# Kernel tuning notes

Hardware: AMD Instinct MI355X
Metric: run time of the kernel (lower is better)

The kernel has to match this reference:

```python
import jax, jax.numpy as jnp
import numpy as np

B, D, N, H = 16, 512, 4096, 4
HD = D // H  # head_dim = 128


def conv1(x, w, b):
    # 1x1 Conv1d == per-position matmul. x: (b, Cin, L), w: (Cout, Cin), b: (Cout,)
    return jnp.einsum('oi,bin->bon', w, x) + b[:, None]


def ln_c(x, g, b, eps=1e-5):
    # TransLN: LayerNorm over the channel axis (axis=1) at every position.
    m = jnp.mean(x, axis=1, keepdims=True)
    v = jnp.var(x, axis=1, keepdims=True)
    return (x - m) * jax.lax.rsqrt(v + eps) * g[:, None] + b[:, None]


def gelu(x):
    return jax.nn.gelu(x, approximate=False)  # torch nn.GELU default = exact erf


def setup_inputs() -> dict:
    key = jax.random.key(0)
    ks = iter(jax.random.split(key, 40))

    def rn(*shape):
        return jax.random.normal(next(ks), shape, jnp.float32) * 0.02

    inp = {
        'group_token': jax.random.normal(next(ks), (B, D, 2), jnp.float32),
        'x': jax.random.normal(next(ks), (B, D, N), jnp.float32),
        # mlp_s: Mlp(2, D//2) -> Conv1d(2, D//2), GELU, Conv1d(D//2, 2)
        'ws1_w': rn(D // 2, 2), 'ws1_b': jnp.zeros(D // 2, jnp.float32),
        'ws2_w': rn(2, D // 2), 'ws2_b': jnp.zeros(2, jnp.float32),
        # mlp_c: Mlp(D, 4D)
        'wc1_w': rn(4 * D, D), 'wc1_b': jnp.zeros(4 * D, jnp.float32),
        'wc2_w': rn(D, 4 * D), 'wc2_b': jnp.zeros(D, jnp.float32),
        # proj q/k/v: Conv1d(D, D)
        'q_w': rn(D, D), 'q_b': jnp.zeros(D, jnp.float32),
        'k_w': rn(D, D), 'k_b': jnp.zeros(D, jnp.float32),
        'v_w': rn(D, D), 'v_b': jnp.zeros(D, jnp.float32),
        'merge_w': rn(D, D), 'merge_b': jnp.zeros(D, jnp.float32),
        # mlp = MLP([2D, 2D, D], do_bn=False): Conv1d(2D,2D), GELU, Conv1d(2D,D)
        'm1_w': rn(2 * D, 2 * D), 'm1_b': jnp.zeros(2 * D, jnp.float32),
        'm2_w': rn(D, 2 * D), 'm2_b': jnp.zeros(D, jnp.float32),
        # norm0 / norm1 LayerNorm(D)
        'n0_g': jnp.ones(D, jnp.float32), 'n0_b': jnp.zeros(D, jnp.float32),
        'n1_g': jnp.ones(D, jnp.float32), 'n1_b': jnp.zeros(D, jnp.float32),
        # grouping: D->64->16->4->2 with TransLN+GELU between, softmax(axis=1)
        'g1_w': rn(64, D), 'g1_b': jnp.zeros(64, jnp.float32),
        'gl1_g': jnp.ones(64, jnp.float32), 'gl1_b': jnp.zeros(64, jnp.float32),
        'g2_w': rn(16, 64), 'g2_b': jnp.zeros(16, jnp.float32),
        'gl2_g': jnp.ones(16, jnp.float32), 'gl2_b': jnp.zeros(16, jnp.float32),
        'g3_w': rn(4, 16), 'g3_b': jnp.zeros(4, jnp.float32),
        'gl3_g': jnp.ones(4, jnp.float32), 'gl3_b': jnp.zeros(4, jnp.float32),
        'g4_w': rn(2, 4), 'g4_b': jnp.zeros(2, jnp.float32),
    }
    return inp


def reference(group_token, x, ws1_w, ws1_b, ws2_w, ws2_b, wc1_w, wc1_b, wc2_w, wc2_b,
              q_w, q_b, k_w, k_b, v_w, v_b, merge_w, merge_b,
              m1_w, m1_b, m2_w, m2_b, n0_g, n0_b, n1_g, n1_b,
              g1_w, g1_b, gl1_g, gl1_b, g2_w, g2_b, gl2_g, gl2_b,
              g3_w, g3_b, gl3_g, gl3_b, g4_w, g4_b):
    b = x.shape[0]
    # group_token: (b, D, 2)
    gt_t = jnp.swapaxes(group_token, 1, 2)                    # (b, 2, D)
    s = conv1(gelu(conv1(gt_t, ws1_w, ws1_b)), ws2_w, ws2_b)  # (b, 2, D)
    gt = group_token + jnp.swapaxes(s, 1, 2)
    gt = gt + conv1(gelu(conv1(gt, wc1_w, wc1_b)), wc2_w, wc2_b)

    # projections; torch view(b, head_dim, heads, -1) splits channels as (HD, H)
    q = conv1(x, q_w, q_b).reshape(b, HD, H, N)
    k = conv1(gt, k_w, k_b).reshape(b, HD, H, 2)
    v = conv1(gt, v_w, v_b).reshape(b, HD, H, 2)

    attn = jax.nn.softmax(jnp.einsum('bdhn,bdhm->bhnm', q, k) * (HD ** -0.5), axis=-1)
    out = jnp.einsum('bhnm,bdhm->bdhn', attn, v).reshape(b, D, N)
    out = conv1(out, merge_w, merge_b)

    h = jnp.concatenate([x, ln_c(out, n0_g, n0_b)], axis=1)   # (b, 2D, N)
    h = conv1(gelu(conv1(h, m1_w, m1_b)), m2_w, m2_b)         # (b, D, N)
    xd = x + ln_c(h, n1_g, n1_b)

    g = gelu(ln_c(conv1(xd, g1_w, g1_b), gl1_g, gl1_b))
    g = gelu(ln_c(conv1(g, g2_w, g2_b), gl2_g, gl2_b))
    g = gelu(ln_c(conv1(g, g3_w, g3_b), gl3_g, gl3_b))
    g = jax.nn.softmax(conv1(g, g4_w, g4_b), axis=1)          # (b, 2, N)
    return g[:, 0, :]                                         # (b, N)
```

## Files before the change

### kernel.cpp

```cpp
#include <hip/hip_runtime.h>
#include <math.h>

typedef unsigned short u16;
typedef unsigned int u32;
typedef __attribute__((ext_vector_type(8))) short bfrag;
typedef __attribute__((ext_vector_type(4))) float f32x4;

__device__ __forceinline__ float gelu_f(float x){
  float z = fabsf(x) * 0.70710678118654752440f;
  float t = __builtin_amdgcn_rcpf(1.0f + 0.3275911f*z);
  float p = t*(0.254829592f + t*(-0.284496736f + t*(1.421413741f
            + t*(-1.453152027f + t*1.061405429f))));
  float e = __expf(-z*z);
  float er = copysignf(1.0f - p*e, x);
  return 0.5f * x * (1.0f + er);
}
__device__ __forceinline__ u16 f2bf(float f){
  union { float f; unsigned int i; } c; c.f = f;
  unsigned int i = c.i;
  return (u16)((i + 0x7FFFu + ((i >> 16) & 1u)) >> 16);
}
__device__ __forceinline__ float bf2f(u16 u){
  union { unsigned int i; float f; } c; c.i = ((unsigned int)u) << 16; return c.f;
}

__device__ __forceinline__ void gload_lds16(const u16* g, u16* l){
  __builtin_amdgcn_global_load_lds(
      (const __attribute__((address_space(1))) u32*)(g),
      (__attribute__((address_space(3))) u32*)(l),
      16, 0, 0);
}

struct F8 { float v[8]; };
__device__ __forceinline__ F8 load8f(const float* p){
  float4 a = *(const float4*)p; float4 b = *(const float4*)(p + 4);
  F8 r; r.v[0]=a.x; r.v[1]=a.y; r.v[2]=a.z; r.v[3]=a.w;
  r.v[4]=b.x; r.v[5]=b.y; r.v[6]=b.z; r.v[7]=b.w; return r;
}

#define PRE_STRIDE 4624

__global__ __launch_bounds__(256) void k0a_mlps(
    const float* __restrict__ gtok,
    const float* __restrict__ ws1_w, const float* __restrict__ ws1_b,
    const float* __restrict__ ws2_w, const float* __restrict__ ws2_b,
    float* __restrict__ GT1)
{
  __shared__ float sw1[256][2]; __shared__ float sb1[256];
  __shared__ float sw2[2][256];
  const int b = blockIdx.x;
  const int t = threadIdx.x;
  sw1[t][0] = ws1_w[2*t]; sw1[t][1] = ws1_w[2*t+1];
  sb1[t] = ws1_b[t];
  sw2[0][t] = ws2_w[t]; sw2[1][t] = ws2_w[256+t];
  __syncthreads();
  const int j = blockIdx.y*256 + t;
  const float a0 = gtok[b*1024 + 2*j], a1 = gtok[b*1024 + 2*j + 1];
  float s0 = ws2_b[0], s1 = ws2_b[1];
  #pragma unroll 4
  for (int o = 0; o < 256; ++o){
    float h = gelu_f(sw1[o][0]*a0 + sw1[o][1]*a1 + sb1[o]);
    s0 += sw2[0][o]*h; s1 += sw2[1][o]*h;
  }
  GT1[b*1024 + 2*j]     = a0 + s0;
  GT1[b*1024 + 2*j + 1] = a1 + s1;
}

__global__ __launch_bounds__(256) void k0b_fc1(
    const float* __restrict__ GT1,
    const float* __restrict__ wc1_w, const float* __restrict__ wc1_b,
    float* __restrict__ HID)
{
  __shared__ float g[1024];
  const int b = blockIdx.x;
  const int t = threadIdx.x;
  for (int i = t; i < 1024; i += 256) g[i] = GT1[b*1024 + i];
  __syncthreads();
  const int o = blockIdx.y*256 + t;
  const float* wr = wc1_w + (size_t)o*512;
  float acc0 = wc1_b[o], acc1 = acc0;
  for (int d = 0; d < 512; d += 8){
    F8 w = load8f(wr + d);
    #pragma unroll
    for (int i = 0; i < 8; ++i){
      acc0 += w.v[i]*g[(d+i)*2];
      acc1 += w.v[i]*g[(d+i)*2+1];
    }
  }
  HID[b*4096 + o]        = gelu_f(acc0);
  HID[b*4096 + 2048 + o] = gelu_f(acc1);
}

__global__ __launch_bounds__(256) void k0c_fc2(
    const float* __restrict__ GT1, const float* __restrict__ HID,
    const float* __restrict__ wc2_w, const float* __restrict__ wc2_b,
    float* __restrict__ GT2)
{
  __shared__ float h0[2048], h1[2048];
  const int b = blockIdx.x;
  const int t = threadIdx.x;
  for (int i = t; i < 2048; i += 256){
    h0[i] = HID[b*4096 + i]; h1[i] = HID[b*4096 + 2048 + i];
  }
  __syncthreads();
  const int d = blockIdx.y*256 + t;
  const float* wr = wc2_w + (size_t)d*2048;
  float acc0 = wc2_b[d], acc1 = acc0;
  for (int o = 0; o < 2048; o += 8){
    F8 w = load8f(wr + o);
    #pragma unroll
    for (int i = 0; i < 8; ++i){
      acc0 += w.v[i]*h0[o+i];
      acc1 += w.v[i]*h1[o+i];
    }
  }
  GT2[b*1024 + 2*d]     = GT1[b*1024 + 2*d]     + acc0;
  GT2[b*1024 + 2*d + 1] = GT1[b*1024 + 2*d + 1] + acc1;
}

__global__ __launch_bounds__(256) void k0d_kv(
    const float* __restrict__ GT2,
    const float* __restrict__ k_w,
    const float* __restrict__ v_w, const float* __restrict__ v_b,
    float* __restrict__ DK, float* __restrict__ DV, float* __restrict__ V1L)
{
  __shared__ float g[1024];
  const int b = blockIdx.x;
  const int t = threadIdx.x;
  for (int i = t; i < 1024; i += 256) g[i] = GT2[b*1024 + i];
  __syncthreads();
  const int c = blockIdx.y*256 + t;
  const float* kr = k_w + (size_t)c*512;
  const float* vr = v_w + (size_t)c*512;
  float k0a=0.f,k1a=0.f,v0a=0.f,v1a=0.f;
  for (int d = 0; d < 512; d += 8){
    F8 kw = load8f(kr + d); F8 vw = load8f(vr + d);
    #pragma unroll
    for (int i = 0; i < 8; ++i){
      float g0 = g[(d+i)*2], g1 = g[(d+i)*2+1];
      k0a += kw.v[i]*g0; k1a += kw.v[i]*g1;
      v0a += vw.v[i]*g0; v1a += vw.v[i]*g1;
    }
  }
  DK[b*512 + c]  = k0a - k1a;
  DV[b*512 + c]  = v0a - v1a;
  V1L[b*512 + c] = v1a + v_b[c];
}

__global__ __launch_bounds__(256) void k0e_qpre(
    const float* __restrict__ DK,
    const float* __restrict__ q_w, const float* __restrict__ q_b,
    float* __restrict__ PRE)
{
  __shared__ float dkl[512];
  const int b = blockIdx.x;
  const int t = threadIdx.x;
  for (int i = t; i < 512; i += 256) dkl[i] = DK[b*512 + i];
  __syncthreads();
  const int i = blockIdx.y*256 + t;
  float w0=0.f,w1=0.f,w2=0.f,w3=0.f;
  for (int c = 0; c < 512; c += 4){
    w0 += dkl[c]  *q_w[(size_t)(c)  *512 + i];
    w1 += dkl[c+1]*q_w[(size_t)(c+1)*512 + i];
    w2 += dkl[c+2]*q_w[(size_t)(c+2)*512 + i];
    w3 += dkl[c+3]*q_w[(size_t)(c+3)*512 + i];
  }
  float* P = PRE + (size_t)b * PRE_STRIDE;
  P[0*512+i]=w0; P[1*512+i]=w1; P[2*512+i]=w2; P[3*512+i]=w3;
  if (blockIdx.y == 0 && t < 4){
    float bsum = 0.f;
    for (int c = t; c < 512; c += 4) bsum += dkl[c]*q_b[c];
    P[2048 + t] = bsum;
  }
}

__global__ __launch_bounds__(256) void k0f_mpre(
    const float* __restrict__ DV, const float* __restrict__ V1L,
    const float* __restrict__ merge_w, const float* __restrict__ merge_b,
    float* __restrict__ PRE)
{
  __shared__ float dvl[512], v1ll[512];
  const int b = blockIdx.x;
  const int t = threadIdx.x;
  for (int i = t; i < 512; i += 256){
    dvl[i] = DV[b*512 + i]; v1ll[i] = V1L[b*512 + i];
  }
  __syncthreads();
  const int r = blockIdx.y*256 + t;
  const float* mw = merge_w + (size_t)r*512;
  float ab = merge_b[r];
  float mh[4] = {0.f,0.f,0.f,0.f};
  for (int c = 0; c < 512; c += 8){
    F8 w = load8f(mw + c);
    #pragma unroll
    for (int i = 0; i < 8; ++i){
      ab += w.v[i]*v1ll[c+i];
      mh[i&3] += w.v[i]*dvl[c+i];
    }
  }
  float* P = PRE + (size_t)b * PRE_STRIDE;
  P[2064 + r] = ab;
  *(float4*)&P[2576 + r*4] = make_float4(mh[0],mh[1],mh[2],mh[3]);
}

__global__ __launch_bounds__(256) void kcvt(const float* __restrict__ s,
                                            u16* __restrict__ d, int n8)
{
  int g = blockIdx.x*256 + threadIdx.x;
  if (g >= n8) return;
  F8 v = load8f(s + (size_t)g*8);
  u16 o[8];
  #pragma unroll
  for (int i=0;i<8;++i) o[i] = f2bf(v.v[i]);
  *(uint4*)(d + (size_t)g*8) = *(uint4*)o;
}

__global__ __launch_bounds__(256) void kcvt_dup(const float* __restrict__ g1w,
                                                u16* __restrict__ out)
{
  int idx = blockIdx.x*256 + threadIdx.x;
  int r = idx >> 10, k = idx & 1023;
  out[idx] = f2bf(g1w[r*512 + (k & 511)]);
}

__global__ __launch_bounds__(256) void k1_fused(
    const float* __restrict__ x, const float* __restrict__ PRE,
    const float* __restrict__ n0_g, const float* __restrict__ n0_b,
    int j0_global, u16* __restrict__ XYbT)
{
  __shared__ float wd[4][512];
  __shared__ float bs[512];
  __shared__ float Mm[512][4];
  __shared__ float gam[512], bet[512];
  __shared__ float beta4[4];
  __shared__ float part[4][4][64];
  __shared__ float pstat[2][4][64];
  const int tid = threadIdx.x;
  const int cid = tid & 63;
  const int qtr = tid >> 6;
  const int jl = blockIdx.x*64 + cid;
  const int jg = j0_global + jl;
  const int b = jg >> 12, n = jg & 4095;
  const float* P = PRE + (size_t)b * PRE_STRIDE;
  for (int i = tid; i < 2048; i += 256) wd[i>>9][i&511] = P[i];
  if (tid < 4) beta4[tid] = P[2048 + tid];
  for (int i = tid; i < 512; i += 256){
    bs[i] = P[2064 + i]; gam[i] = n0_g[i]; bet[i] = n0_b[i];
  }
  for (int i = tid; i < 2048; i += 256) Mm[i>>2][i&3] = P[2576 + i];
  __syncthreads();
  const float* xc = x + (size_t)b*2097152 + n;
  u16* col = XYbT + (size_t)jl*1024;
  const int ibase = qtr*128;
  float l0=0.f, l1=0.f, l2=0.f, l3=0.f;
  for (int i0 = 0; i0 < 128; i0 += 32){
    u16 ob[32];
    #pragma unroll
    for (int m = 0; m < 32; ++m){
      int i = ibase + i0 + m;
      float xv = xc[(size_t)i*4096];
      ob[m] = f2bf(xv);
      l0 += wd[0][i]*xv; l1 += wd[1][i]*xv;
      l2 += wd[2][i]*xv; l3 += wd[3][i]*xv;
    }
    #pragma unroll
    for (int q = 0; q < 4; ++q)
      *(uint4*)&col[ibase + i0 + 8*q] = *(uint4*)&ob[8*q];
  }
  part[0][qtr][cid] = l0; part[1][qtr][cid] = l1;
  part[2][qtr][cid] = l2; part[3][qtr][cid] = l3;
  __syncthreads();
  l0 = part[0][0][cid] + part[0][1][cid] + part[0][2][cid] + part[0][3][cid] + beta4[0];
  l1 = part[1][0][cid] + part[1][1][cid] + part[1][2][cid] + part[1][3][cid] + beta4[1];
  l2 = part[2][0][cid] + part[2][1][cid] + part[2][2][cid] + part[2][3][cid] + beta4[2];
  l3 = part[3][0][cid] + part[3][1][cid] + part[3][2][cid] + part[3][3][cid] + beta4[3];
  const float sc = 0.0883883476483184405f;
  float p0 = 1.f/(1.f+expf(-sc*l0));
  float p1 = 1.f/(1.f+expf(-sc*l1));
  float p2 = 1.f/(1.f+expf(-sc*l2));
  float p3 = 1.f/(1.f+expf(-sc*l3));
  float s=0.f, s2=0.f;
  for (int c = ibase; c < ibase + 128; ++c){
    float m = bs[c] + Mm[c][0]*p0 + Mm[c][1]*p1 + Mm[c][2]*p2 + Mm[c][3]*p3;
    s += m; s2 += m*m;
  }
  pstat[0][qtr][cid] = s; pstat[1][qtr][cid] = s2;
  __syncthreads();
  s  = pstat[0][0][cid] + pstat[0][1][cid] + pstat[0][2][cid] + pstat[0][3][cid];
  s2 = pstat[1][0][cid] + pstat[1][1][cid] + pstat[1][2][cid] + pstat[1][3][cid];
  float mean = s*(1.f/512.f);
  float rs = rsqrtf(s2*(1.f/512.f) - mean*mean + 1e-5f);
  for (int c0 = 0; c0 < 128; c0 += 32){
    u16 ob[32];
    #pragma unroll
    for (int m = 0; m < 32; ++m){
      int c = ibase + c0 + m;
      float v = bs[c] + Mm[c][0]*p0 + Mm[c][1]*p1 + Mm[c][2]*p2 + Mm[c][3]*p3;
      ob[m] = f2bf((v - mean)*rs*gam[c] + bet[c]);
    }
    #pragma unroll
    for (int q = 0; q < 4; ++q)
      *(uint4*)&col[512 + ibase + c0 + 8*q] = *(uint4*)&ob[8*q];
  }
}

__global__ __launch_bounds__(256) void mfma_gemm_p(
    const u16* __restrict__ Wb, const float* __restrict__ bias,
    const u16* __restrict__ XT, int K, int M,
    u16* __restrict__ Out, int do_gelu, int log2nbi)
{
  __shared__ __align__(16) u16 SH[3][8192];
  const int tid = threadIdx.x;
  const int lane = tid & 63;
  const int wv = __builtin_amdgcn_readfirstlane(tid >> 6);
  const int id = blockIdx.x;
  const int bi = (id >> 3) & ((1 << log2nbi) - 1);
  const int bj = (id & 7) + 8 * (id >> (3 + log2nbi));
  const int roff = (wv >> 1) * 64;
  const int noff = (wv & 1) * 64;
  const int lm = lane & 15, quad = lane >> 4;
  const int qs = (quad ^ ((lm >> 1) & 3)) * 8;

  f32x4 acc[4][4];
  #pragma unroll
  for (int i=0;i<4;++i){
    #pragma unroll
    for (int j=0;j<4;++j) acc[i][j] = (f32x4){0.f,0.f,0.f,0.f};
  }

  const int r16 = lane >> 2;
  const int kc  = (((lane & 3) ^ ((lane >> 3) & 3))) * 8;
  const u16* aG = Wb + (size_t)(bi*128 + wv*32 + r16)*K + kc;
  const u16* bG = XT + (size_t)(bj*128 + wv*32 + r16)*1024 + kc;
  const int aOff = wv*1024;
  const int bOff = 4096 + wv*1024;

#define GP_STAGE(base, kk) do { \
    gload_lds16(aG + (kk),                 (base) + aOff); \
    gload_lds16(aG + (size_t)16*K + (kk),  (base) + aOff + 512); \
    gload_lds16(bG + (kk),                 (base) + bOff); \
    gload_lds16(bG + 16*1024 + (kk),       (base) + bOff + 512); \
  } while(0)

#define GP_COMPUTE(base) do { \
    bfrag av[4], bv[4]; \
    _Pragma("unroll") \
    for (int i=0;i<4;++i) \
      av[i] = *(const bfrag*)&(base)[(roff + 16*i + lm)*32 + qs]; \
    _Pragma("unroll") \
    for (int j=0;j<4;++j) \
      bv[j] = *(const bfrag*)&(base)[4096 + (noff + 16*j + lm)*32 + qs]; \
    __builtin_amdgcn_s_setprio(1); \
    _Pragma("unroll") \
    for (int i=0;i<4;++i){ \
      _Pragma("unroll") \
      for (int j=0;j<4;++j) \
        acc[i][j] = __builtin_amdgcn_mfma_f32_16x16x32_bf16(av[i], bv[j], acc[i][j], 0,0,0); \
    } \
    __builtin_amdgcn_s_setprio(0); \
  } while(0)

  u16* b0 = &SH[0][0];
  u16* b1 = &SH[1][0];
  u16* b2 = &SH[2][0];
  GP_STAGE(b0, 0);
  GP_STAGE(b1, 32);
  for (int k0 = 0; k0 + 64 < K; k0 += 32){
    GP_STAGE(b2, k0 + 64);
    asm volatile("s_waitcnt vmcnt(8)" ::: "memory");
    __builtin_amdgcn_s_barrier();
    __builtin_amdgcn_sched_barrier(0);
    GP_COMPUTE(b0);
    __builtin_amdgcn_sched_barrier(0);
    __builtin_amdgcn_s_barrier();
    u16* t = b0; b0 = b1; b1 = b2; b2 = t;
  }
  asm volatile("s_waitcnt vmcnt(4)" ::: "memory");
  __builtin_amdgcn_s_barrier();
  __builtin_amdgcn_sched_barrier(0);
  GP_COMPUTE(b0);
  asm volatile("s_waitcnt vmcnt(0)" ::: "memory");
  __builtin_amdgcn_s_barrier();
  __builtin_amdgcn_sched_barrier(0);
  GP_COMPUTE(b1);
  __syncthreads();
#undef GP_STAGE
#undef GP_COMPUTE

  u16* Tt = &SH[0][0];
  #pragma unroll
  for (int i=0;i<4;++i){
    float4 bb = *(const float4*)&bias[bi*128 + roff + 16*i + quad*4];
    float b4[4] = {bb.x,bb.y,bb.z,bb.w};
    #pragma unroll
    for (int j=0;j<4;++j){
      int colr = noff + 16*j + lm;
      #pragma unroll
      for (int s2=0;s2<2;++s2){
        float v0 = acc[i][j][2*s2]   + b4[2*s2];
        float v1 = acc[i][j][2*s2+1] + b4[2*s2+1];
        if (do_gelu){ v0 = gelu_f(v0); v1 = gelu_f(v1); }
        unsigned int dw = (unsigned int)f2bf(v0) | ((unsigned int)f2bf(v1) << 16);
        *(unsigned int*)&Tt[colr*136 + roff + 16*i + quad*4 + 2*s2] = dw;
      }
    }
  }
  __syncthreads();
  {
    int c = tid >> 1, q = tid & 1;
    u16* dst = Out + (size_t)(bj*128 + c)*M + bi*128 + q*64;
    const u16* src = &Tt[c*136 + q*64];
    #pragma unroll
    for (int m=0;m<8;++m)
      *(uint4*)(dst + m*8) = *(const uint4*)(src + m*8);
  }
}

__global__ __launch_bounds__(256) void mfma_g64h(
    const u16* __restrict__ Wg, const float* __restrict__ bias,
    const u16* __restrict__ XT,
    const float* __restrict__ gl1_g, const float* __restrict__ gl1_b,
    const float* __restrict__ g2_w, const float* __restrict__ g2_b,
    const float* __restrict__ gl2_g, const float* __restrict__ gl2_b,
    const float* __restrict__ g3_w, const float* __restrict__ g3_b,
    const float* __restrict__ gl3_g, const float* __restrict__ gl3_b,
    const float* __restrict__ g4_w, const float* __restrict__ g4_b, int has_g4b,
    float* __restrict__ Outp, int j0_global)
{
  __shared__ __align__(16) u16 SH[3][6144];
  const int tid = threadIdx.x;
  const int lane = tid & 63;
  const int wv = __builtin_amdgcn_readfirstlane(tid >> 6);
  const int bj = blockIdx.x;
  const int lm = lane & 15, quad = lane >> 4;
  const int qs = (quad ^ ((lm >> 1) & 3)) * 8;

  f32x4 acc[4][2];
  #pragma unroll
  for (int i=0;i<4;++i){
    #pragma unroll
    for (int j=0;j<2;++j) acc[i][j] = (f32x4){0.f,0.f,0.f,0.f};
  }
  const int r16 = lane >> 2;
  const int kc  = (((lane & 3) ^ ((lane >> 3) & 3))) * 8;
  const u16* aG = Wg + (size_t)(wv*16 + r16)*1024 + kc;
  const u16* bG = XT + (size_t)(bj*128 + wv*32 + r16)*1024 + kc;
  const int aOff = wv*512;
  const int bOff = 2048 + wv*1024;

#define G64_STAGE(base, kk) do { \
    gload_lds16(aG + (kk),             (base) + aOff); \
    gload_lds16(bG + (kk),             (base) + bOff); \
    gload_lds16(bG + 16*1024 + (kk),   (base) + bOff + 512); \
  } while(0)

#define G64_COMPUTE(base) do { \
    bfrag av[4], bv[2]; \
    _Pragma("unroll") \
    for (int i=0;i<4;++i) \
      av[i] = *(const bfrag*)&(base)[(16*i + lm)*32 + qs]; \
    _Pragma("unroll") \
    for (int j=0;j<2;++j) \
      bv[j] = *(const bfrag*)&(base)[2048 + (wv*32 + 16*j + lm)*32 + qs]; \
    __builtin_amdgcn_s_setprio(1); \
    _Pragma("unroll") \
    for (int i=0;i<4;++i){ \
      _Pragma("unroll") \
      for (int j=0;j<2;++j) \
        acc[i][j] = __builtin_amdgcn_mfma_f32_16x16x32_bf16(av[i], bv[j], acc[i][j], 0,0,0); \
    } \
    __builtin_amdgcn_s_setprio(0); \
  } while(0)

  u16* b0 = &SH[0][0];
  u16* b1 = &SH[1][0];
  u16* b2 = &SH[2][0];
  G64_STAGE(b0, 0);
  G64_STAGE(b1, 32);
  for (int k0 = 0; k0 + 64 < 1024; k0 += 32){
    G64_STAGE(b2, k0 + 64);
    asm volatile("s_waitcnt vmcnt(6)" ::: "memory");
    __builtin_amdgcn_s_barrier();
    __builtin_amdgcn_sched_barrier(0);
    G64_COMPUTE(b0);
    __builtin_amdgcn_sched_barrier(0);
    __builtin_amdgcn_s_barrier();
    u16* t = b0; b0 = b1; b1 = b2; b2 = t;
  }
  asm volatile("s_waitcnt vmcnt(3)" ::: "memory");
  __builtin_amdgcn_s_barrier();
  __builtin_amdgcn_sched_barrier(0);
  G64_COMPUTE(b0);
  asm volatile("s_waitcnt vmcnt(0)" ::: "memory");
  __builtin_amdgcn_s_barrier();
  __builtin_amdgcn_sched_barrier(0);
  G64_COMPUTE(b1);
  __syncthreads();
#undef G64_STAGE
#undef G64_COMPUTE

  u16* Tg = &SH[0][0];
  #pragma unroll
  for (int i=0;i<4;++i){
    float4 bb = *(const float4*)&bias[16*i + quad*4];
    float b4[4] = {bb.x,bb.y,bb.z,bb.w};
    #pragma unroll
    for (int j=0;j<2;++j){
      int col = wv*32 + 16*j + lm;
      #pragma unroll
      for (int s2=0;s2<2;++s2){
        float v0 = acc[i][j][2*s2]   + b4[2*s2];
        float v1 = acc[i][j][2*s2+1] + b4[2*s2+1];
        unsigned int dw = (unsigned int)f2bf(v0) | ((unsigned int)f2bf(v1) << 16);
        *(unsigned int*)&Tg[col*72 + 16*i + quad*4 + 2*s2] = dw;
      }
    }
  }
  float* HW = (float*)(&SH[0][0] + 9216);
  if (tid < 64){ HW[tid] = gl1_g[tid]; HW[64+tid] = gl1_b[tid]; }
  for (int i = tid; i < 1024; i += 256) HW[128+i] = g2_w[i];
  if (tid < 16){ HW[1152+tid]=g2_b[tid]; HW[1168+tid]=gl2_g[tid]; HW[1184+tid]=gl2_b[tid]; }
  if (tid >= 64 && tid < 128) HW[1200 + tid-64] = g3_w[tid-64];
  if (tid >= 128 && tid < 132){
    int q = tid - 128;
    HW[1264+q]=g3_b[q]; HW[1268+q]=gl3_g[q]; HW[1272+q]=gl3_b[q];
    HW[1276+q] = g4_w[q] - g4_w[4+q];
  }
  if (tid == 132) HW[1280] = has_g4b ? (g4_b[0] - g4_b[1]) : 0.f;
  __syncthreads();

  if (tid < 128){
    const u16* gc = &Tg[tid*72];
    float a1[64]; float s=0.f;
    #pragma unroll
    for (int c0=0;c0<64;c0+=8){
      uint4 w = *(const uint4*)(gc + c0);
      const u16* wp = (const u16*)&w;
      #pragma unroll
      for (int m=0;m<8;++m){ a1[c0+m] = bf2f(wp[m]); s += a1[c0+m]; }
    }
    float m = s*(1.f/64.f); float s2=0.f;
    #pragma unroll
    for (int c=0;c<64;++c){ float d=a1[c]-m; s2+=d*d; }
    float rs = rsqrtf(s2*(1.f/64.f)+1e-5f);
    #pragma unroll
    for (int c=0;c<64;++c) a1[c] = gelu_f((a1[c]-m)*rs*HW[c]+HW[64+c]);

    float a2[16]; s=0.f;
    #pragma unroll
    for (int i=0;i<16;++i){
      float acc2 = HW[1152+i];
      #pragma unroll
      for (int o=0;o<64;++o) acc2 += HW[128 + i*64 + o]*a1[o];
      a2[i]=acc2; s+=acc2;
    }
    m = s*(1.f/16.f); s2=0.f;
    #pragma unroll
    for (int i=0;i<16;++i){ float d=a2[i]-m; s2+=d*d; }
    rs = rsqrtf(s2*(1.f/16.f)+1e-5f);
    float a2g[16];
    #pragma unroll
    for (int i=0;i<16;++i) a2g[i] = gelu_f((a2[i]-m)*rs*HW[1168+i]+HW[1184+i]);

    float a3[4]; s=0.f;
    #pragma unroll
    for (int i=0;i<4;++i){
      float acc3 = HW[1264+i];
      #pragma unroll
      for (int o=0;o<16;++o) acc3 += HW[1200 + i*16 + o]*a2g[o];
      a3[i]=acc3; s+=acc3;
    }
    m = s*0.25f; s2=0.f;
    #pragma unroll
    for (int i=0;i<4;++i){ float d=a3[i]-m; s2+=d*d; }
    rs = rsqrtf(s2*0.25f+1e-5f);
    float z = HW[1280];
    #pragma unroll
    for (int i=0;i<4;++i) z += HW[1276+i]*gelu_f((a3[i]-m)*rs*HW[1268+i]+HW[1272+i]);
    Outp[j0_global + bj*128 + tid] = 1.f/(1.f+expf(-z));
  }
}

__global__ __launch_bounds__(256) void k_lnT(
    const u16* __restrict__ t2T,
    const float* __restrict__ gamma, const float* __restrict__ beta,
    u16* __restrict__ XYbT)
{
  __shared__ float gam[512], bet[512];
  const int tid = threadIdx.x;
  for (int c = tid; c < 512; c += 256){ gam[c]=gamma[c]; bet[c]=beta[c]; }
  __syncthreads();
  const int lane = tid & 63, wv = tid >> 6;
  const int j = blockIdx.x*4 + wv;
  uint4 w = *(const uint4*)(t2T + (size_t)j*512 + lane*8);
  const u16* wp = (const u16*)&w;
  float vv[8];
  #pragma unroll
  for (int m=0;m<8;++m) vv[m] = bf2f(wp[m]);
  float s = 0.f, s2 = 0.f;
  #pragma unroll
  for (int m=0;m<8;++m){ s += vv[m]; s2 += vv[m]*vv[m]; }
  #pragma unroll
  for (int off = 32; off; off >>= 1){
    s  += __shfl_xor(s,  off, 64);
    s2 += __shfl_xor(s2, off, 64);
  }
  float mean = s*(1.f/512.f);
  float rs = rsqrtf(s2*(1.f/512.f) - mean*mean + 1e-5f);
  u16 ob[8];
  #pragma unroll
  for (int m=0;m<8;++m){
    int c = lane*8 + m;
    ob[m] = f2bf((vv[m]-mean)*rs*gam[c] + bet[c]);
  }
  *(uint4*)&XYbT[(size_t)j*1024 + 512 + lane*8] = *(uint4*)ob;
}

extern "C" void kernel_launch(void* const* d_in, const int* in_sizes, int n_in,
                              void* d_out, int out_size, void* d_ws, size_t ws_size,
                              hipStream_t stream)
{
  const float* gtok  = (const float*)d_in[0];
  const float* x     = (const float*)d_in[1];
  const float* ws1_w = (const float*)d_in[2];
  const float* ws1_b = (const float*)d_in[3];
  const float* ws2_w = (const float*)d_in[4];
  const float* ws2_b = (const float*)d_in[5];
  const float* wc1_w = (const float*)d_in[6];
  const float* wc1_b = (const float*)d_in[7];
  const float* wc2_w = (const float*)d_in[8];
  const float* wc2_b = (const float*)d_in[9];
  const float* q_w   = (const float*)d_in[10];
  const float* q_b   = (const float*)d_in[11];
  const float* k_w   = (const float*)d_in[12];
  const float* v_w   = (const float*)d_in[14];
  const float* v_b   = (const float*)d_in[15];
  const float* merge_w = (const float*)d_in[16];
  const float* merge_b = (const float*)d_in[17];
  const float* m1_w  = (const float*)d_in[18];
  const float* m1_b  = (const float*)d_in[19];
  const float* m2_w  = (const float*)d_in[20];
  const float* m2_b  = (const float*)d_in[21];
  const float* n0_g  = (const float*)d_in[22];
  const float* n0_b  = (const float*)d_in[23];
  const float* n1_g  = (const float*)d_in[24];
  const float* n1_b  = (const float*)d_in[25];
  const float* g1_w  = (const float*)d_in[26];
  const float* g1_b  = (const float*)d_in[27];
  const float* gl1_g = (const float*)d_in[28];
  const float* gl1_b = (const float*)d_in[29];
  const float* g2_w  = (const float*)d_in[30];
  const float* g2_b  = (const float*)d_in[31];
  const float* gl2_g = (const float*)d_in[32];
  const float* gl2_b = (const float*)d_in[33];
  const float* g3_w  = (const float*)d_in[34];
  const float* g3_b  = (const float*)d_in[35];
  const float* gl3_g = (const float*)d_in[36];
  const float* gl3_b = (const float*)d_in[37];
  const float* g4_w  = (const float*)d_in[38];
  const float* g4_b  = (n_in > 39) ? (const float*)d_in[39] : nullptr;

  const int TOT = 65536;
  const size_t PRE_BYTES = (size_t)16 * PRE_STRIDE * 4;
  const size_t GT1_B = 65536, HID_B = 262144, GT2_B = 65536;
  const size_t DK_B = 32768, DV_B = 32768, V1L_B = 32768;
  const size_t WB1_B = (size_t)1024*1024*2;
  const size_t WB2_B = (size_t)512*1024*2;
  const size_t WG_B  = (size_t)64*1024*2;
  const size_t FIXED = PRE_BYTES + GT1_B + HID_B + GT2_B + DK_B + DV_B + V1L_B
                     + WB1_B + WB2_B + WG_B;
  int C = 65536;
  while (C > 4096 && FIXED + (size_t)5120*C > ws_size) C >>= 1;
  const int nch = TOT / C;

  char* wsb = (char*)d_ws;
  size_t off = 0;
  float* PRE = (float*)(wsb + off); off += PRE_BYTES;
  float* GT1 = (float*)(wsb + off); off += GT1_B;
  float* HID = (float*)(wsb + off); off += HID_B;
  float* GT2 = (float*)(wsb + off); off += GT2_B;
  float* DK  = (float*)(wsb + off); off += DK_B;
  float* DV  = (float*)(wsb + off); off += DV_B;
  float* V1L = (float*)(wsb + off); off += V1L_B;
  u16* Wb1   = (u16*)(wsb + off);   off += WB1_B;
  u16* Wb2   = (u16*)(wsb + off);   off += WB2_B;
  u16* Wg    = (u16*)(wsb + off);   off += WG_B;
  u16* XYbT  = (u16*)(wsb + off);   off += (size_t)2048*C;
  u16* T1bT  = (u16*)(wsb + off);   off += (size_t)2048*C;
  u16* T2bT  = (u16*)(wsb + off);   off += (size_t)1024*C;

  dim3 blk(256);
  hipLaunchKernelGGL(kcvt, dim3(512), blk, 0, stream, m1_w, Wb1, 1024*1024/8);
  hipLaunchKernelGGL(kcvt, dim3(256), blk, 0, stream, m2_w, Wb2, 512*1024/8);
  hipLaunchKernelGGL(kcvt_dup, dim3(256), blk, 0, stream, g1_w, Wg);
  hipLaunchKernelGGL(k0a_mlps, dim3(16,2), blk, 0, stream,
      gtok, ws1_w, ws1_b, ws2_w, ws2_b, GT1);
  hipLaunchKernelGGL(k0b_fc1, dim3(16,8), blk, 0, stream, GT1, wc1_w, wc1_b, HID);
  hipLaunchKernelGGL(k0c_fc2, dim3(16,2), blk, 0, stream, GT1, HID, wc2_w, wc2_b, GT2);
  hipLaunchKernelGGL(k0d_kv,  dim3(16,2), blk, 0, stream, GT2, k_w, v_w, v_b, DK, DV, V1L);
  hipLaunchKernelGGL(k0e_qpre, dim3(16,2), blk, 0, stream, DK, q_w, q_b, PRE);
  hipLaunchKernelGGL(k0f_mpre, dim3(16,2), blk, 0, stream, DV, V1L, merge_w, merge_b, PRE);

  for (int ch = 0; ch < nch; ++ch){
    const int j0 = ch * C;
    hipLaunchKernelGGL(k1_fused, dim3(C/64), blk, 0, stream,
        x, PRE, n0_g, n0_b, j0, XYbT);
    hipLaunchKernelGGL(mfma_gemm_p, dim3(8*(C/128)), blk, 0, stream,
        Wb1, m1_b, XYbT, 1024, 1024, T1bT, 1, 3);
    hipLaunchKernelGGL(mfma_gemm_p, dim3(4*(C/128)), blk, 0, stream,
        Wb2, m2_b, T1bT, 1024, 512, T2bT, 0, 2);
    hipLaunchKernelGGL(k_lnT, dim3(C/4), blk, 0, stream, T2bT, n1_g, n1_b, XYbT);
    hipLaunchKernelGGL(mfma_g64h, dim3(C/128), blk, 0, stream,
        Wg, g1_b, XYbT,
        gl1_g, gl1_b, g2_w, g2_b, gl2_g, gl2_b,
        g3_w, g3_b, gl3_g, gl3_b,
        g4_w, g4_b ? g4_b : g4_w, g4_b ? 1 : 0, (float*)d_out, j0);
  }
}
```

Before: 891.7 us.

## Double-buffer GEMM main loop with 64-wide K steps across four LDS stages

Restructures the mfma_gemm_p pipeline from a triple-buffered 32-wide K loop to four LDS buffers processed in pairs, so each iteration computes two 32-wide slices per barrier pair and then refills both. Global pointers are advanced incrementally instead of recomputed from offsets. The aim is to halve barrier count per K and increase the work between waits. In exchange, LDS use per block grows from 48KB to 64KB, which may lower occupancy, and K must be a multiple of 64 with at least 128.

```diff
diff --git a/kernel.cpp b/kernel.cpp
--- a/kernel.cpp
+++ b/kernel.cpp
@@ -309,7 +309,7 @@
     const u16* __restrict__ XT, int K, int M,
     u16* __restrict__ Out, int do_gelu, int log2nbi)
 {
-  __shared__ __align__(16) u16 SH[3][8192];
+  __shared__ __align__(16) u16 SH[4][8192];
   const int tid = threadIdx.x;
   const int lane = tid & 63;
   const int wv = __builtin_amdgcn_readfirstlane(tid >> 6);
@@ -330,16 +330,19 @@
 
   const int r16 = lane >> 2;
   const int kc  = (((lane & 3) ^ ((lane >> 3) & 3))) * 8;
-  const u16* aG = Wb + (size_t)(bi*128 + wv*32 + r16)*K + kc;
-  const u16* bG = XT + (size_t)(bj*128 + wv*32 + r16)*1024 + kc;
+  const u16* pa0 = Wb + (size_t)(bi*128 + wv*32 + r16)*K + kc;
+  const u16* pa1 = pa0 + (size_t)16*K;
+  const u16* pb0 = XT + (size_t)(bj*128 + wv*32 + r16)*1024 + kc;
+  const u16* pb1 = pb0 + 16*1024;
   const int aOff = wv*1024;
   const int bOff = 4096 + wv*1024;
 
-#define GP_STAGE(base, kk) do { \
-    gload_lds16(aG + (kk),                 (base) + aOff); \
-    gload_lds16(aG + (size_t)16*K + (kk),  (base) + aOff + 512); \
-    gload_lds16(bG + (kk),                 (base) + bOff); \
-    gload_lds16(bG + 16*1024 + (kk),       (base) + bOff + 512); \
+#define GP_STAGE(base) do { \
+    gload_lds16(pa0, (base) + aOff); \
+    gload_lds16(pa1, (base) + aOff + 512); \
+    gload_lds16(pb0, (base) + bOff); \
+    gload_lds16(pb1, (base) + bOff + 512); \
+    pa0 += 32; pa1 += 32; pb0 += 32; pb1 += 32; \
   } while(0)
 
 #define GP_COMPUTE(base) do { \
@@ -360,29 +363,37 @@
     __builtin_amdgcn_s_setprio(0); \
   } while(0)
 
-  u16* b0 = &SH[0][0];
-  u16* b1 = &SH[1][0];
-  u16* b2 = &SH[2][0];
-  GP_STAGE(b0, 0);
-  GP_STAGE(b1, 32);
-  for (int k0 = 0; k0 + 64 < K; k0 += 32){
-    GP_STAGE(b2, k0 + 64);
+  u16* cA = &SH[0][0];
+  u16* cB = &SH[1][0];
+  u16* nA = &SH[2][0];
+  u16* nB = &SH[3][0];
+  GP_STAGE(cA); GP_STAGE(cB);
+  GP_STAGE(nA); GP_STAGE(nB);
+  const int NIT = (K >> 6) - 2;
+  for (int it = 0; it < NIT; ++it){
     asm volatile("s_waitcnt vmcnt(8)" ::: "memory");
     __builtin_amdgcn_s_barrier();
     __builtin_amdgcn_sched_barrier(0);
-    GP_COMPUTE(b0);
+    GP_COMPUTE(cA);
+    GP_COMPUTE(cB);
     __builtin_amdgcn_sched_barrier(0);
     __builtin_amdgcn_s_barrier();
-    u16* t = b0; b0 = b1; b1 = b2; b2 = t;
-  }
-  asm volatile("s_waitcnt vmcnt(4)" ::: "memory");
+    __builtin_amdgcn_sched_barrier(0);
+    GP_STAGE(cA); GP_STAGE(cB);
+    u16* t;
+    t = cA; cA = nA; nA = t;
+    t = cB; cB = nB; nB = t;
+  }
+  asm volatile("s_waitcnt vmcnt(8)" ::: "memory");
   __builtin_amdgcn_s_barrier();
   __builtin_amdgcn_sched_barrier(0);
-  GP_COMPUTE(b0);
+  GP_COMPUTE(cA);
+  GP_COMPUTE(cB);
   asm volatile("s_waitcnt vmcnt(0)" ::: "memory");
   __builtin_amdgcn_s_barrier();
   __builtin_amdgcn_sched_barrier(0);
-  GP_COMPUTE(b1);
+  GP_COMPUTE(nA);
+  GP_COMPUTE(nB);
   __syncthreads();
 #undef GP_STAGE
 #undef GP_COMPUTE
```

Result: slower. 916.9 us (+2.8%).
